# Kernel tuning notes

Measured on AMD Instinct MI355X. Metric: run time of the kernel, lower is better.

The kernel has to match this reference:

```python
import jax, jax.numpy as jnp
import numpy as np

MAX_DISP = 4  # PWC-Net correlation: displacements in [-4,4] -> 9x9 = 81 channels


def setup_inputs() -> dict:
    key = jax.random.key(0)
    k1, k2 = jax.random.split(key)
    B, C, H, W = 8, 128, 112, 192
    tensorFirst = jax.random.normal(k1, (B, C, H, W), dtype=jnp.float32)
    tensorSecond = jax.random.normal(k2, (B, C, H, W), dtype=jnp.float32)
    return {"tensorFirst": tensorFirst, "tensorSecond": tensorSecond}


def reference(tensorFirst, tensorSecond):
    B, C, H, W = tensorFirst.shape
    D = MAX_DISP
    # zero-pad second by max displacement on each spatial side (rbot padding of 8 = 2*4)
    padded = jnp.pad(tensorSecond, ((0, 0), (0, 0), (D, D), (D, D)))
    outs = []
    # fixed 9x9 displacement grid; channel index = (dy+4)*9 + (dx+4)
    for dy in range(2 * D + 1):
        for dx in range(2 * D + 1):
            shifted = jax.lax.dynamic_slice(padded, (0, 0, dy, dx), (B, C, H, W))
            # dot product over channels, normalized by C (sumelems in the cupy kernel)
            outs.append(jnp.mean(tensorFirst * shifted, axis=1))
    return jnp.stack(outs, axis=1)  # [B, 81, H, W]
```

## Files before the change

kernel.cpp:

```cpp
#include <hip/hip_runtime.h>


namespace {
constexpr int kC = 128;
constexpr int kH = 112;
constexpr int kW = 192;
constexpr int kD = 4;
constexpr int kKD = 9;
constexpr int kHW = kH * kW;
constexpr long long kCHW = (long long)kC * kHW;

constexpr int PX = 8;
constexpr int XG = kW / PX;
constexpr int YT = 8;
constexpr int NT = XG * YT;
}

__device__ __attribute__((aligned(16))) float g_zeros[4] = {0.f, 0.f, 0.f, 0.f};

__global__ __launch_bounds__(NT, 4)
void corr81_kernel(const float* __restrict__ first,
                   const float* __restrict__ second,
                   float* __restrict__ out) {
  const int g = blockIdx.x;
  const int b = g & 7;
  const int i = g >> 3;
  const int dy = i % kKD;
  const int y0 = (i / kKD) * YT;

  const int tid = threadIdx.x;
  const int xg = tid % XG;
  const int yl = tid / XG;
  const int px0 = xg * PX;
  const int y = y0 + yl;
  const int ys = y + dy - kD;

  float acc[PX][kKD];
#pragma unroll
  for (int p = 0; p < PX; ++p)
#pragma unroll
    for (int d = 0; d < kKD; ++d) acc[p][d] = 0.0f;

  if ((unsigned)ys < (unsigned)kH) {
    const bool left = (xg == 0);
    const bool right = (xg == XG - 1);

    const float* fp = first + (long long)b * kCHW + (long long)y * kW + px0;
    const float* sp = second + (long long)b * kCHW + (long long)ys * kW + px0;
    const float* pw0 = left ? g_zeros : (sp - 4);
    const float* pw3 = right ? g_zeros : (sp + 8);
    const long long st0 = left ? 0 : kHW;
    const long long st3 = right ? 0 : kHW;

    for (int c = 0; c < kC; ++c) {
      const float4 f0 = *(const float4*)(fp);
      const float4 f1 = *(const float4*)(fp + 4);
      const float4 w0 = *(const float4*)(pw0);
      const float4 w1 = *(const float4*)(sp);
      const float4 w2 = *(const float4*)(sp + 4);
      const float4 w3 = *(const float4*)(pw3);

      const float fa[PX] = {f0.x, f0.y, f0.z, f0.w, f1.x, f1.y, f1.z, f1.w};
      const float sw[16] = {w0.x, w0.y, w0.z, w0.w, w1.x, w1.y, w1.z, w1.w,
                            w2.x, w2.y, w2.z, w2.w, w3.x, w3.y, w3.z, w3.w};
#pragma unroll
      for (int p = 0; p < PX; ++p)
#pragma unroll
        for (int d = 0; d < kKD; ++d)
          acc[p][d] = fmaf(fa[p], sw[p + d], acc[p][d]);

      fp += kHW;
      sp += kHW;
      pw0 += st0;
      pw3 += st3;
    }
  }

  const float scale = 1.0f / (float)kC;
  float* obase = out + ((long long)b * 81 + (long long)dy * kKD) * kHW +
                 (long long)y * kW + px0;
#pragma unroll
  for (int d = 0; d < kKD; ++d) {
    float4 o0 = make_float4(acc[0][d] * scale, acc[1][d] * scale,
                            acc[2][d] * scale, acc[3][d] * scale);
    float4 o1 = make_float4(acc[4][d] * scale, acc[5][d] * scale,
                            acc[6][d] * scale, acc[7][d] * scale);
    float* op = obase + (long long)d * kHW;
    *(float4*)op = o0;
    *(float4*)(op + 4) = o1;
  }
}

extern "C" void kernel_launch(void* const* d_in, const int* in_sizes, int n_in,
                              void* d_out, int out_size, void* d_ws, size_t ws_size,
                              hipStream_t stream) {
  const float* first = (const float*)d_in[0];
  const float* second = (const float*)d_in[1];
  float* out = (float*)d_out;

  const int grid = 8 * (kH / YT) * kKD;
  corr81_kernel<<<grid, NT, 0, stream>>>(first, second, out);
}
```

Before: 331.2 us.

## Compute correlation with bf16 MFMA over LDS-staged tiles

```diff
diff --git a/kernel.cpp b/kernel.cpp
--- a/kernel.cpp
+++ b/kernel.cpp
@@ -1,94 +1,143 @@
 #include <hip/hip_runtime.h>
 
 
+typedef __attribute__((ext_vector_type(8))) short bf16x8;
+typedef __attribute__((ext_vector_type(4))) float f32x4;
+
 namespace {
-constexpr int kC = 128;
-constexpr int kH = 112;
-constexpr int kW = 192;
-constexpr int kD = 4;
-constexpr int kKD = 9;
+constexpr int kC = 128, kH = 112, kW = 192;
 constexpr int kHW = kH * kW;
 constexpr long long kCHW = (long long)kC * kHW;
-
-constexpr int PX = 8;
-constexpr int XG = kW / PX;
 constexpr int YT = 8;
-constexpr int NT = XG * YT;
+constexpr int XT = 16;
+constexpr int NS = 32;
+constexpr int YS = 16;
+constexpr int KC = 32;
+constexpr int NT = 384;
+constexpr int A_YSTRIDE = XT * KC * 2;
+constexpr int B_YSTRIDE = NS * KC * 2;
+constexpr int B_OFF = YT * A_YSTRIDE;
+constexpr int LDS_BYTES = B_OFF + YS * B_YSTRIDE;
+constexpr int A_SLOTS = YT * XT * (KC / 8);
+constexpr int B_SLOTS = YS * NS * (KC / 8);
 }
 
-__device__ __attribute__((aligned(16))) float g_zeros[4] = {0.f, 0.f, 0.f, 0.f};
+__device__ __forceinline__ unsigned pack2_bf16(float a, float b) {
+  unsigned ua = __float_as_uint(a) + 0x8000u;
+  unsigned ub = __float_as_uint(b) + 0x8000u;
+  return (ua >> 16) | (ub & 0xffff0000u);
+}
 
-__global__ __launch_bounds__(NT, 4)
-void corr81_kernel(const float* __restrict__ first,
-                   const float* __restrict__ second,
-                   float* __restrict__ out) {
+__global__ __launch_bounds__(NT, 3)
+void corr81_mfma(const float* __restrict__ first,
+                 const float* __restrict__ second,
+                 float* __restrict__ out) {
+  __shared__ uint4 lds4[LDS_BYTES / 16];
+  unsigned char* lds = (unsigned char*)lds4;
+
   const int g = blockIdx.x;
   const int b = g & 7;
   const int i = g >> 3;
-  const int dy = i % kKD;
-  const int y0 = (i / kKD) * YT;
+  const int xt = i % (kW / XT);
+  const int yt = i / (kW / XT);
+  const int x0 = xt * XT, y0 = yt * YT;
 
   const int tid = threadIdx.x;
-  const int xg = tid % XG;
-  const int yl = tid / XG;
-  const int px0 = xg * PX;
-  const int y = y0 + yl;
-  const int ys = y + dy - kD;
+  const int lane = tid & 63;
+  const int wv = tid >> 6;
+  const int dy_w = (wv % 3) * 3;
+  const int y_w = (wv / 3) * 4;
+  const int col = lane & 15;
+  const int q = lane >> 4;
 
-  float acc[PX][kKD];
+  f32x4 acc[4][3][2];
 #pragma unroll
-  for (int p = 0; p < PX; ++p)
+  for (int yy = 0; yy < 4; ++yy)
 #pragma unroll
-    for (int d = 0; d < kKD; ++d) acc[p][d] = 0.0f;
+    for (int dd = 0; dd < 3; ++dd)
+#pragma unroll
+      for (int nh = 0; nh < 2; ++nh) acc[yy][dd][nh] = (f32x4){0.f, 0.f, 0.f, 0.f};
 
-  if ((unsigned)ys < (unsigned)kH) {
-    const bool left = (xg == 0);
-    const bool right = (xg == XG - 1);
+  const float* fb = first + (long long)b * kCHW;
+  const float* sb = second + (long long)b * kCHW;
 
-    const float* fp = first + (long long)b * kCHW + (long long)y * kW + px0;
-    const float* sp = second + (long long)b * kCHW + (long long)ys * kW + px0;
-    const float* pw0 = left ? g_zeros : (sp - 4);
-    const float* pw3 = right ? g_zeros : (sp + 8);
-    const long long st0 = left ? 0 : kHW;
-    const long long st3 = right ? 0 : kHW;
+  for (int ck = 0; ck < kC / KC; ++ck) {
+    const int c0 = ck * KC;
+    __syncthreads();
 
-    for (int c = 0; c < kC; ++c) {
-      const float4 f0 = *(const float4*)(fp);
-      const float4 f1 = *(const float4*)(fp + 4);
-      const float4 w0 = *(const float4*)(pw0);
-      const float4 w1 = *(const float4*)(sp);
-      const float4 w2 = *(const float4*)(sp + 4);
-      const float4 w3 = *(const float4*)(pw3);
+    for (int s = tid; s < A_SLOTS + B_SLOTS; s += NT) {
+      if (s < A_SLOTS) {
+        const int kg = s & 3, xl = (s >> 2) & 15, yl = s >> 6;
+        const float* p = fb + (long long)(c0 + kg * 8) * kHW +
+                         (y0 + yl) * kW + (x0 + xl);
+        uint4 w;
+        w.x = pack2_bf16(p[0], p[kHW]);
+        w.y = pack2_bf16(p[2 * kHW], p[3 * kHW]);
+        w.z = pack2_bf16(p[4 * kHW], p[5 * kHW]);
+        w.w = pack2_bf16(p[6 * kHW], p[7 * kHW]);
+        *(uint4*)(lds + yl * A_YSTRIDE + xl * (KC * 2) + kg * 16) = w;
+      } else {
+        const int t = s - A_SLOTS;
+        const int kg = t & 3, n = (t >> 2) & 31, ys = t >> 7;
+        const int ysg = y0 + ys - 4;
+        const int xsg = x0 + n - 4;
+        uint4 w = make_uint4(0u, 0u, 0u, 0u);
+        if ((unsigned)ysg < (unsigned)kH && (unsigned)xsg < (unsigned)kW) {
+          const float* p = sb + (long long)(c0 + kg * 8) * kHW +
+                           ysg * kW + xsg;
+          w.x = pack2_bf16(p[0], p[kHW]);
+          w.y = pack2_bf16(p[2 * kHW], p[3 * kHW]);
+          w.z = pack2_bf16(p[4 * kHW], p[5 * kHW]);
+          w.w = pack2_bf16(p[6 * kHW], p[7 * kHW]);
+        }
+        *(uint4*)(lds + B_OFF + ys * B_YSTRIDE + n * (KC * 2) + kg * 16) = w;
+      }
+    }
+    __syncthreads();
 
-      const float fa[PX] = {f0.x, f0.y, f0.z, f0.w, f1.x, f1.y, f1.z, f1.w};
-      const float sw[16] = {w0.x, w0.y, w0.z, w0.w, w1.x, w1.y, w1.z, w1.w,
-                            w2.x, w2.y, w2.z, w2.w, w3.x, w3.y, w3.z, w3.w};
+    bf16x8 aF[4];
 #pragma unroll
-      for (int p = 0; p < PX; ++p)
+    for (int yy = 0; yy < 4; ++yy)
+      aF[yy] = *(const bf16x8*)(lds + (y_w + yy) * A_YSTRIDE + col * (KC * 2) +
+                                q * 16);
+    const int sbase = y_w + dy_w;
 #pragma unroll
-        for (int d = 0; d < kKD; ++d)
-          acc[p][d] = fmaf(fa[p], sw[p + d], acc[p][d]);
-
-      fp += kHW;
-      sp += kHW;
-      pw0 += st0;
-      pw3 += st3;
+    for (int nh = 0; nh < 2; ++nh) {
+      bf16x8 bF[6];
+#pragma unroll
+      for (int si = 0; si < 6; ++si)
+        bF[si] = *(const bf16x8*)(lds + B_OFF + (sbase + si) * B_YSTRIDE +
+                                  (nh * 16 + col) * (KC * 2) + q * 16);
+#pragma unroll
+      for (int yy = 0; yy < 4; ++yy)
+#pragma unroll
+        for (int dd = 0; dd < 3; ++dd)
+          acc[yy][dd][nh] = __builtin_amdgcn_mfma_f32_16x16x32_bf16(
+              aF[yy], bF[yy + dd], acc[yy][dd][nh], 0, 0, 0);
     }
   }
 
-  const float scale = 1.0f / (float)kC;
-  float* obase = out + ((long long)b * 81 + (long long)dy * kKD) * kHW +
-                 (long long)y * kW + px0;
+  const float scale = 1.f / 128.f;
 #pragma unroll
-  for (int d = 0; d < kKD; ++d) {
-    float4 o0 = make_float4(acc[0][d] * scale, acc[1][d] * scale,
-                            acc[2][d] * scale, acc[3][d] * scale);
-    float4 o1 = make_float4(acc[4][d] * scale, acc[5][d] * scale,
-                            acc[6][d] * scale, acc[7][d] * scale);
-    float* op = obase + (long long)d * kHW;
-    *(float4*)op = o0;
-    *(float4*)(op + 4) = o1;
-  }
+  for (int nh = 0; nh < 2; ++nh)
+#pragma unroll
+    for (int r = 0; r < 4; ++r) {
+      const int xloc = q * 4 + r;
+      const int d = nh * 16 + col - xloc;
+      if ((unsigned)d <= 8u) {
+#pragma unroll
+        for (int yy = 0; yy < 4; ++yy)
+#pragma unroll
+          for (int dd = 0; dd < 3; ++dd) {
+            const int ch = (dy_w + dd) * 9 + d;
+            const long long o =
+                (((long long)b * 81 + ch) * kH + (y0 + y_w + yy)) *
+                    (long long)kW +
+                (x0 + xloc);
+            out[o] = acc[yy][dd][nh][r] * scale;
+          }
+      }
+    }
 }
 
 extern "C" void kernel_launch(void* const* d_in, const int* in_sizes, int n_in,
@@ -98,6 +147,6 @@
   const float* second = (const float*)d_in[1];
   float* out = (float*)d_out;
 
-  const int grid = 8 * (kH / YT) * kKD;
-  corr81_kernel<<<grid, NT, 0, stream>>>(first, second, out);
+  const int grid = 8 * (kH / YT) * (kW / XT);
+  corr81_mfma<<<grid, NT, 0, stream>>>(first, second, out);
 }
```

After: 334.0 us. No clear change (+0.8%).
